# Kernel tuning notes

Hardware: AMD Instinct MI355X
Metric: run time of the kernel (lower is better)

The kernel has to match this reference:

```python
import jax, jax.numpy as jnp
import numpy as np

N = 50000      # nodes
E = 800000     # edges (avg degree 16)
NF, EF, H, OUT, K = 16, 8, 64, 8, 3
N_MID = 2      # n_gnn_layers=4 -> first + 2 mid + last


def setup_inputs() -> dict:
    key = jax.random.key(0)
    ks = jax.random.split(key, 16)
    s = 0.05
    return {
        "x": jax.random.normal(ks[0], (N, NF), dtype=jnp.float32),
        "edge_index": jax.random.randint(ks[1], (2, E), 0, N, dtype=jnp.int64),
        "edge_attr": jax.random.normal(ks[2], (E, EF), dtype=jnp.float32),
        # edge_aggr MLP: Linear(EF,H) -> ReLU -> Linear(H,1)
        "mlp_W1": jax.random.normal(ks[3], (EF, H), dtype=jnp.float32) * s,
        "mlp_b1": jnp.zeros((H,), dtype=jnp.float32),
        "mlp_W2": jax.random.normal(ks[4], (H, 1), dtype=jnp.float32) * s,
        "mlp_b2": jnp.zeros((1,), dtype=jnp.float32),
        # TAGConv-style layers: K+1 linear maps each
        "W_first": jax.random.normal(ks[5], (K + 1, NF, H), dtype=jnp.float32) * s,
        "b_first": jnp.zeros((H,), dtype=jnp.float32),
        "W_mid": jax.random.normal(ks[6], (N_MID, K + 1, H, H), dtype=jnp.float32) * s,
        "b_mid": jnp.zeros((N_MID, H), dtype=jnp.float32),
        "W_last": jax.random.normal(ks[7], (K + 1, H, OUT), dtype=jnp.float32) * s,
        "b_last": jnp.zeros((OUT,), dtype=jnp.float32),
    }


def _gcn_norm(edge_weight, src, dst, n_nodes):
    # deg computed at target (col), D^{-1/2} A D^{-1/2}, no self loops
    deg = jax.ops.segment_sum(edge_weight, dst, num_segments=n_nodes)
    dinv = jnp.where(deg > 0, jax.lax.rsqrt(jnp.where(deg > 0, deg, 1.0)), 0.0)
    return dinv[src] * edge_weight * dinv[dst]  # [E]


def _tag_conv(x, Ws, b, src, dst, norm, n_nodes):
    # out = sum_k (A_norm^k x) W_k + b
    out = x @ Ws[0]
    h = x
    for k in range(1, Ws.shape[0]):
        h = jax.ops.segment_sum(h[src] * norm[:, None], dst, num_segments=n_nodes)
        out = out + h @ Ws[k]
    return out + b


def reference(x, edge_index, edge_attr, mlp_W1, mlp_b1, mlp_W2, mlp_b2,
              W_first, b_first, W_mid, b_mid, W_last, b_last):
    src, dst = edge_index[0], edge_index[1]
    n_nodes = x.shape[0]
    # edge MLP -> scalar edge weight per edge
    ew = (jax.nn.relu(edge_attr @ mlp_W1 + mlp_b1) @ mlp_W2 + mlp_b2)[:, 0]  # [E]
    norm = _gcn_norm(ew, src, dst, n_nodes)
    h = jax.nn.relu(_tag_conv(x, W_first, b_first, src, dst, norm, n_nodes))
    for i in range(W_mid.shape[0]):
        h = jax.nn.relu(_tag_conv(h, W_mid[i], b_mid[i], src, dst, norm, n_nodes))
    return _tag_conv(h, W_last, b_last, src, dst, norm, n_nodes)
```

## Files before the change

kernel.cpp:

```cpp
#include <hip/hip_runtime.h>
#include <stdint.h>

#define N_NODES 50000
#define N_EDGES 800000
#define NFEAT   16
#define EFEAT   8
#define HID     64
#define OUTF    8
#define NMID    2
#define NX      (N_NODES * NFEAT)
#define NPW     16
#define CAP     64
#define PGB     ((N_NODES + 4 * NPW - 1) / (4 * NPW))
#define PPB     ((N_NODES + 15) / 16)
#define NWB     ((N_NODES + 3) / 4)

typedef unsigned short ushort_t;
typedef unsigned int   uint_t;
typedef unsigned long long ull_t;
typedef __bf16 bf16x8 __attribute__((ext_vector_type(8)));
typedef float  f32x4  __attribute__((ext_vector_type(4)));

__device__ __forceinline__ float b2f(ushort_t u) {
    return __uint_as_float(((uint_t)u) << 16);
}
__device__ __forceinline__ ushort_t f2b(float f) {
    uint_t u = __float_as_uint(f);
    return (ushort_t)((u + 0x7fffu + ((u >> 16) & 1u)) >> 16);
}
__device__ __forceinline__ float h2f(ushort_t u) {
    union { ushort_t u; _Float16 h; } c; c.u = u; return (float)c.h;
}
__device__ __forceinline__ ushort_t f2h(float f) {
    union { ushort_t u; _Float16 h; } c; c.h = (_Float16)f; return c.u;
}

__global__ __launch_bounds__(256) void edge_mlp_kernel(
    const float* __restrict__ ea, const float* __restrict__ x,
    const int* __restrict__ ei,
    const float* __restrict__ W1, const float* __restrict__ b1,
    const float* __restrict__ W2, const float* __restrict__ b2,
    ushort_t* __restrict__ xb, float* __restrict__ ew,
    int* __restrict__ cnts, uint_t* __restrict__ bucket)
{
    __shared__ float W1s[EFEAT * HID];
    __shared__ float b1s[HID];
    __shared__ float W2s[HID];
    __shared__ float b2s;
    int tid = threadIdx.x;
    for (int i = tid; i < EFEAT * HID; i += 256) W1s[i] = W1[i];
    if (tid < HID) { b1s[tid] = b1[tid]; W2s[tid] = W2[tid]; }
    if (tid == 0) b2s = b2[0];
    __syncthreads();

    int e = blockIdx.x * 256 + tid;
    if (e >= N_EDGES) return;

    xb[e] = f2b(x[e]);

    float4 v0 = ((const float4*)ea)[2 * e];
    float4 v1 = ((const float4*)ea)[2 * e + 1];
    float a[8] = {v0.x, v0.y, v0.z, v0.w, v1.x, v1.y, v1.z, v1.w};

    float acc = b2s;
    #pragma unroll 4
    for (int j = 0; j < HID; ++j) {
        float h = b1s[j];
        #pragma unroll
        for (int i = 0; i < EFEAT; ++i) h = fmaf(a[i], W1s[i * HID + j], h);
        acc = fmaf(fmaxf(h, 0.f), W2s[j], acc);
    }
    ew[e] = acc;

    int d = ei[N_EDGES + e];
    int pos = atomicAdd(&cnts[d], 1);
    if (pos < CAP)
        bucket[(size_t)d * CAP + pos] = (uint_t)e;
}

__global__ __launch_bounds__(256) void degdinv_kernel(
    int* __restrict__ cnts, const uint_t* __restrict__ bucket,
    const float* __restrict__ ew, float* __restrict__ dinv)
{
    int tid = threadIdx.x;
    int n = blockIdx.x * 4 + (tid >> 6);
    int lane = tid & 63;
    if (n >= N_NODES) return;
    int c = cnts[n]; if (c > CAP) c = CAP;
    float w = 0.f;
    if (lane < c)
        w = ew[bucket[(size_t)n * CAP + lane]];
    #pragma unroll
    for (int o = 32; o; o >>= 1) w += __shfl_down(w, o, 64);
    if (lane == 0) {
        cnts[n] = c;
        dinv[n] = (w > 0.f) ? (1.f / sqrtf(w)) : 0.f;
    }
}

__global__ __launch_bounds__(256) void rescale_kernel(
    const int* __restrict__ cnts, const float* __restrict__ dinv,
    const float* __restrict__ ew, const int* __restrict__ ei,
    uint_t* __restrict__ bucket)
{
    int tid = threadIdx.x;
    int n = blockIdx.x * 4 + (tid >> 6);
    int lane = tid & 63;
    if (n >= N_NODES) return;
    int c = cnts[n];
    float dn = dinv[n];
    if (lane < c) {
        uint_t e = bucket[(size_t)n * CAP + lane];
        int s = ei[e];
        float nv = dinv[s] * ew[e] * dn;
        nv = fminf(fmaxf(nv, -60000.f), 60000.f);
        bucket[(size_t)n * CAP + lane] = (((uint_t)f2h(nv)) << 16) | (uint_t)s;
    }
}

template<int W>
__global__ __launch_bounds__(256, 6) void prop_kernel(
    const ushort_t* __restrict__ gsrc, ushort_t* __restrict__ gout,
    const int* __restrict__ cnts, const uint_t* __restrict__ bucket)
{
    int tid = threadIdx.x;
    int wv = tid >> 6, lane = tid & 63;
    int nb = (blockIdx.x * 4 + wv) * 4;
    if (nb >= N_NODES) return;

    int cv = (lane < 4) ? cnts[nb + lane] : 0;
    int c0 = __builtin_amdgcn_readlane(cv, 0);
    int c1 = __builtin_amdgcn_readlane(cv, 1);
    int c2 = __builtin_amdgcn_readlane(cv, 2);
    int c3 = __builtin_amdgcn_readlane(cv, 3);

    uint_t p0 = 0, p1 = 0, p2 = 0, p3 = 0;
    if (lane < c0) p0 = bucket[(size_t)(nb + 0) * CAP + lane];
    if (lane < c1) p1 = bucket[(size_t)(nb + 1) * CAP + lane];
    if (lane < c2) p2 = bucket[(size_t)(nb + 2) * CAP + lane];
    if (lane < c3) p3 = bucket[(size_t)(nb + 3) * CAP + lane];

    if (W == 64) {
        float s[4][4];
        #pragma unroll
        for (int n = 0; n < 4; ++n)
            #pragma unroll
            for (int k = 0; k < 4; ++k) s[n][k] = 0.f;

        int cq0 = c0 & ~3, cq1 = c1 & ~3, cq2 = c2 & ~3, cq3 = c3 & ~3;
        int cqm = max(max(cq0, cq1), max(cq2, cq3));

        for (int j = 0; j < cqm; j += 4) {
            #define GATHER4(pN, cqN, n)                                              \
                if (j < cqN) {                                                       \
                    _Pragma("unroll")                                                \
                    for (int k = 0; k < 4; ++k) {                                    \
                        int pe = __builtin_amdgcn_readlane((int)pN, j + k);          \
                        float nv = h2f((ushort_t)(((uint_t)pe) >> 16));              \
                        float h = b2f(gsrc[(size_t)(pe & 0xffff) * 64 + lane]);      \
                        s[n][k] = fmaf(h, nv, s[n][k]);                              \
                    }                                                                \
                }
            GATHER4(p0, cq0, 0)
            GATHER4(p1, cq1, 1)
            GATHER4(p2, cq2, 2)
            GATHER4(p3, cq3, 3)
            #undef GATHER4
        }
        #define TAIL(pN, cqN, cN, n)                                                 \
            for (int j = cqN; j < cN; ++j) {                                         \
                int pe = __builtin_amdgcn_readlane((int)pN, j);                      \
                float nv = h2f((ushort_t)(((uint_t)pe) >> 16));                      \
                float h = b2f(gsrc[(size_t)(pe & 0xffff) * 64 + lane]);              \
                s[n][0] = fmaf(h, nv, s[n][0]);                                      \
            }
        TAIL(p0, cq0, c0, 0)
        TAIL(p1, cq1, c1, 1)
        TAIL(p2, cq2, c2, 2)
        TAIL(p3, cq3, c3, 3)
        #undef TAIL

        #pragma unroll
        for (int n = 0; n < 4; ++n) {
            float v = (s[n][0] + s[n][1]) + (s[n][2] + s[n][3]);
            gout[(size_t)(nb + n) * 64 + lane] = f2b(v);
        }
    } else {
        const int il = lane & 15;
        const int quad = lane >> 4;
        #define PROC16(pN, cN, n)                                                    \
            {                                                                        \
                float s = 0.f;                                                       \
                for (int j = 0; j < cN; j += 4) {                                    \
                    int j4 = j + quad;                                               \
                    int pw = __shfl((int)pN, j4 & 63, 64);                           \
                    bool valid = j4 < cN;                                            \
                    int src = valid ? (pw & 0xffff) : 0;                             \
                    float nv = valid ? h2f((ushort_t)(((uint_t)pw) >> 16)) : 0.f;    \
                    float h = b2f(gsrc[(size_t)src * 16 + il]);                      \
                    s = fmaf(h, nv, s);                                              \
                }                                                                    \
                s += __shfl_xor(s, 16, 64);                                          \
                s += __shfl_xor(s, 32, 64);                                          \
                if (lane < 16) gout[(size_t)(nb + n) * 16 + lane] = f2b(s);          \
            }
        PROC16(p0, c0, 0)
        PROC16(p1, c1, 1)
        PROC16(p2, c2, 2)
        PROC16(p3, c3, 3)
        #undef PROC16
    }
}

template<int F32OUT>
__global__ __launch_bounds__(256, 8) void prop8_kernel(
    const ushort_t* __restrict__ gsrc, int GS, int GO,
    const ushort_t* __restrict__ add, int AS, int AO,
    ushort_t* __restrict__ outb, float* __restrict__ outf,
    const int* __restrict__ cnts, const uint_t* __restrict__ bucket)
{
    int tid = threadIdx.x;
    int wv = tid >> 6, lane = tid & 63;
    int nb = (blockIdx.x * 4 + wv) * 4;
    if (nb >= N_NODES) return;
    const int oct = lane >> 3, il = lane & 7;

    int cv = (lane < 4) ? cnts[nb + lane] : 0;
    int c0 = __builtin_amdgcn_readlane(cv, 0);
    int c1 = __builtin_amdgcn_readlane(cv, 1);
    int c2 = __builtin_amdgcn_readlane(cv, 2);
    int c3 = __builtin_amdgcn_readlane(cv, 3);

    uint_t p0 = 0, p1 = 0, p2 = 0, p3 = 0;
    if (lane < c0) p0 = bucket[(size_t)(nb + 0) * CAP + lane];
    if (lane < c1) p1 = bucket[(size_t)(nb + 1) * CAP + lane];
    if (lane < c2) p2 = bucket[(size_t)(nb + 2) * CAP + lane];
    if (lane < c3) p3 = bucket[(size_t)(nb + 3) * CAP + lane];

    #define PROC8(pN, cN, n)                                                         \
        {                                                                            \
            float s = 0.f;                                                           \
            for (int j = 0; j < cN; j += 8) {                                        \
                int jo = j + oct;                                                    \
                int pw = __shfl((int)pN, jo & 63, 64);                               \
                bool valid = jo < cN;                                                \
                int src = valid ? (pw & 0xffff) : 0;                                 \
                float nv = valid ? h2f((ushort_t)(((uint_t)pw) >> 16)) : 0.f;        \
                float h = b2f(gsrc[(size_t)src * GS + GO + il]);                     \
                s = fmaf(h, nv, s);                                                  \
            }                                                                        \
            s += __shfl_xor(s, 8, 64);                                               \
            s += __shfl_xor(s, 16, 64);                                              \
            s += __shfl_xor(s, 32, 64);                                              \
            if (lane < 8) {                                                          \
                float v = s + b2f(add[(size_t)(nb + n) * AS + AO + lane]);           \
                if (F32OUT) outf[(size_t)(nb + n) * 8 + lane] = v;                   \
                else        outb[(size_t)(nb + n) * 8 + lane] = f2b(v);              \
            }                                                                        \
        }
    PROC8(p0, c0, 0)
    PROC8(p1, c1, 1)
    PROC8(p2, c2, 2)
    PROC8(p3, c3, 3)
    #undef PROC8
}

template<int SRCW, int COUT, int ACT>
__global__ __launch_bounds__(256, 4) void gemm4_kernel(
    const ushort_t* __restrict__ s0, const ushort_t* __restrict__ s1,
    const ushort_t* __restrict__ s2, const ushort_t* __restrict__ s3,
    const float* __restrict__ Wg,
    const float* __restrict__ bias,
    ushort_t* __restrict__ outb)
{
    constexpr int NCH = (SRCW == 16) ? 2 : 8;
    constexpr int NT  = (COUT + 15) / 16;
    __shared__ __align__(16) ushort_t Bp[NCH * NT * 512];

    int tid = threadIdx.x;
    for (int idx = tid; idx < NCH * NT * 512; idx += 256) {
        int f = idx >> 9;
        int l = (idx >> 3) & 63, j = idx & 7;
        int ch = f / NT, nt = f - ch * NT;
        int kk = ((l >> 4) << 3) + j;
        int n = nt * 16 + (l & 15);
        int widx, krow;
        if (SRCW == 16) { widx = 2 * ch + (kk >> 4); krow = kk & 15; }
        else            { widx = ch >> 1;            krow = ((ch & 1) << 5) + kk; }
        float v = (n < COUT) ? Wg[((size_t)widx * SRCW + krow) * COUT + n] : 0.f;
        Bp[idx] = f2b(v);
    }
    __syncthreads();

    int wv = tid >> 6, lane = tid & 63;
    int node_base = (blockIdx.x * 4 + wv) * NPW;
    if (node_base >= N_NODES) return;
    int m = lane & 15, quad = lane >> 4;

    const ushort_t* srcs[4] = {s0, s1, s2, s3};
    bf16x8 a[NCH];
    #pragma unroll
    for (int ch = 0; ch < NCH; ++ch) {
        const ushort_t* sp;
        size_t off;
        if (SRCW == 16) {
            sp = (quad < 2) ? srcs[2 * ch] : srcs[2 * ch + 1];
            off = (size_t)(node_base + m) * 16 + (quad & 1) * 8;
        } else {
            sp = srcs[ch >> 1];
            off = (size_t)(node_base + m) * 64 + ((ch & 1) << 5) + quad * 8;
        }
        a[ch] = *(const bf16x8*)(sp + off);
    }

    #pragma unroll
    for (int nt = 0; nt < NT; ++nt) {
        float bv = bias[(nt * 16 + m) & (COUT - 1)];
        f32x4 c = {bv, bv, bv, bv};
        #pragma unroll
        for (int ch = 0; ch < NCH; ++ch) {
            bf16x8 b = *(const bf16x8*)&Bp[((ch * NT + nt) * 64 + lane) * 8];
            c = __builtin_amdgcn_mfma_f32_16x16x32_bf16(a[ch], b, c, 0, 0, 0);
        }
        #pragma unroll
        for (int r = 0; r < 4; ++r) {
            int row = node_base + quad * 4 + r;
            float v = ACT ? fmaxf(c[r], 0.f) : c[r];
            outb[(size_t)row * COUT + nt * 16 + m] = f2b(v);
        }
    }
}

__global__ __launch_bounds__(256, 4) void gemmL_kernel(
    const ushort_t* __restrict__ src,
    const float* __restrict__ Wl,
    const float* __restrict__ bl,
    ushort_t* __restrict__ Z)
{
    __shared__ __align__(16) ushort_t Bp[2 * 2 * 512];

    int tid = threadIdx.x;
    for (int idx = tid; idx < 2048; idx += 256) {
        int f = idx >> 9;
        int ch = f >> 1, nt = f & 1;
        int l = (idx >> 3) & 63, j = idx & 7;
        int kg = ch * 32 + ((l >> 4) << 3) + j;
        int n = nt * 16 + (l & 15);
        int widx = n >> 3, col = n & 7;
        Bp[idx] = f2b(Wl[((size_t)widx * 64 + kg) * 8 + col]);
    }
    __syncthreads();

    int wv = tid >> 6, lane = tid & 63;
    int node_base = (blockIdx.x * 4 + wv) * NPW;
    if (node_base >= N_NODES) return;
    int m = lane & 15, quad = lane >> 4;

    bf16x8 a[2];
    #pragma unroll
    for (int ch = 0; ch < 2; ++ch)
        a[ch] = *(const bf16x8*)(src + (size_t)(node_base + m) * 64 + ch * 32 + quad * 8);

    #pragma unroll
    for (int nt = 0; nt < 2; ++nt) {
        int n = nt * 16 + m;
        float bv = (n < 8) ? bl[n] : 0.f;
        f32x4 c = {bv, bv, bv, bv};
        #pragma unroll
        for (int ch = 0; ch < 2; ++ch) {
            bf16x8 b = *(const bf16x8*)&Bp[((ch * 2 + nt) * 64 + lane) * 8];
            c = __builtin_amdgcn_mfma_f32_16x16x32_bf16(a[ch], b, c, 0, 0, 0);
        }
        #pragma unroll
        for (int r = 0; r < 4; ++r) {
            int row = node_base + quad * 4 + r;
            Z[(size_t)row * 32 + n] = f2b(c[r]);
        }
    }
}

extern "C" void kernel_launch(void* const* d_in, const int* in_sizes, int n_in,
                              void* d_out, int out_size, void* d_ws, size_t ws_size,
                              hipStream_t stream)
{
    const float* x  = (const float*)d_in[0];
    const int*   ei = (const int*)d_in[1];
    const float* ea = (const float*)d_in[2];
    const float* W1 = (const float*)d_in[3];
    const float* b1 = (const float*)d_in[4];
    const float* W2 = (const float*)d_in[5];
    const float* b2 = (const float*)d_in[6];
    const float* Wf = (const float*)d_in[7];
    const float* bf = (const float*)d_in[8];
    const float* Wm = (const float*)d_in[9];
    const float* bm = (const float*)d_in[10];
    const float* Wl = (const float*)d_in[11];
    const float* bl = (const float*)d_in[12];

    char* ws = (char*)d_ws;
    size_t off = 0;
    auto take = [&](size_t bytes) -> char* {
        char* p = ws + off;
        off = (off + bytes + 255) & ~(size_t)255;
        return p;
    };
    int*      cnts   = (int*)take((size_t)N_NODES * 4);
    float*    dinv   = (float*)take((size_t)N_NODES * 4);
    float*    ew     = (float*)take((size_t)N_EDGES * 4);
    uint_t*   bucket = (uint_t*)take((size_t)N_NODES * CAP * 4);
    ushort_t* xb     = (ushort_t*)take((size_t)NX * 2 + 256);
    ushort_t* g1     = (ushort_t*)take((size_t)N_NODES * HID * 2 + 256);
    ushort_t* g2     = (ushort_t*)take((size_t)N_NODES * HID * 2 + 256);
    ushort_t* g3     = (ushort_t*)take((size_t)N_NODES * HID * 2 + 256);
    ushort_t* curA   = (ushort_t*)take((size_t)N_NODES * HID * 2 + 256);
    ushort_t* curB   = (ushort_t*)take((size_t)N_NODES * HID * 2 + 256);
    ushort_t* Z      = (ushort_t*)take((size_t)N_NODES * 32 * 2 + 256);
    ushort_t* t8a    = (ushort_t*)take((size_t)N_NODES * 8 * 2 + 256);
    ushort_t* t8b    = (ushort_t*)take((size_t)N_NODES * 8 * 2 + 256);

    hipMemsetAsync(cnts, 0, (size_t)N_NODES * 4, stream);

    const int EB = (N_EDGES + 255) / 256;

    edge_mlp_kernel<<<EB, 256, 0, stream>>>(ea, x, ei, W1, b1, W2, b2, xb, ew, cnts, bucket);
    degdinv_kernel<<<NWB, 256, 0, stream>>>(cnts, bucket, ew, dinv);
    rescale_kernel<<<NWB, 256, 0, stream>>>(cnts, dinv, ew, ei, bucket);

    prop_kernel<NFEAT><<<PPB, 256, 0, stream>>>(xb, g1, cnts, bucket);
    prop_kernel<NFEAT><<<PPB, 256, 0, stream>>>(g1, g2, cnts, bucket);
    prop_kernel<NFEAT><<<PPB, 256, 0, stream>>>(g2, g3, cnts, bucket);
    gemm4_kernel<NFEAT, HID, 1><<<PGB, 256, 0, stream>>>(
        xb, g1, g2, g3, Wf, bf, curA);

    ushort_t* cin = curA;
    ushort_t* cot = curB;
    for (int L = 0; L < NMID; ++L) {
        prop_kernel<HID><<<PPB, 256, 0, stream>>>(cin, g1, cnts, bucket);
        prop_kernel<HID><<<PPB, 256, 0, stream>>>(g1, g2, cnts, bucket);
        prop_kernel<HID><<<PPB, 256, 0, stream>>>(g2, g3, cnts, bucket);
        gemm4_kernel<HID, HID, 1><<<PGB, 256, 0, stream>>>(
            cin, g1, g2, g3, Wm + (size_t)L * 4 * HID * HID, bm + L * HID, cot);
        ushort_t* t = cin; cin = cot; cot = t;
    }

    gemmL_kernel<<<PGB, 256, 0, stream>>>(cin, Wl, bl, Z);
    prop8_kernel<0><<<PPB, 256, 0, stream>>>(Z, 32, 24, Z, 32, 16, t8a, nullptr, cnts, bucket);
    prop8_kernel<0><<<PPB, 256, 0, stream>>>(t8a, 8, 0, Z, 32, 8, t8b, nullptr, cnts, bucket);
    prop8_kernel<1><<<PPB, 256, 0, stream>>>(t8b, 8, 0, Z, 32, 0, nullptr, (float*)d_out, cnts, bucket);
}
```

Baseline: 456.3 us.

## Fuse third mid-layer propagation hop with the 4-way GEMM and transpose edge-MLP weights

For each middle layer, the third propagation hop is fused with the four-term MFMA GEMM into one kernel. The gathered hop-3 features are staged in shared memory instead of being written to and re-read from a global buffer, which removes one kernel launch per layer. The cost is that each block of 16 nodes rebuilds the full 64x256 weight panel in LDS, and the lower occupancy bound may hurt latency hiding for the gather. The edge MLP weights are also transposed so each hidden unit's inputs load as float4 vectors, with the bias and W2 packed into one float2.

```diff
diff --git a/kernel.cpp b/kernel.cpp
--- a/kernel.cpp
+++ b/kernel.cpp
@@ -43,13 +43,15 @@
     ushort_t* __restrict__ xb, float* __restrict__ ew,
     int* __restrict__ cnts, uint_t* __restrict__ bucket)
 {
-    __shared__ float W1s[EFEAT * HID];
-    __shared__ float b1s[HID];
-    __shared__ float W2s[HID];
+    __shared__ __align__(16) float W1t[EFEAT * HID];
+    __shared__ __align__(8)  float2 b1w2[HID];
     __shared__ float b2s;
     int tid = threadIdx.x;
-    for (int i = tid; i < EFEAT * HID; i += 256) W1s[i] = W1[i];
-    if (tid < HID) { b1s[tid] = b1[tid]; W2s[tid] = W2[tid]; }
+    for (int idx = tid; idx < EFEAT * HID; idx += 256) {
+        int j = idx >> 3, i = idx & 7;
+        W1t[idx] = W1[i * HID + j];
+    }
+    if (tid < HID) b1w2[tid] = make_float2(b1[tid], W2[tid]);
     if (tid == 0) b2s = b2[0];
     __syncthreads();
 
@@ -60,15 +62,19 @@
 
     float4 v0 = ((const float4*)ea)[2 * e];
     float4 v1 = ((const float4*)ea)[2 * e + 1];
-    float a[8] = {v0.x, v0.y, v0.z, v0.w, v1.x, v1.y, v1.z, v1.w};
 
     float acc = b2s;
-    #pragma unroll 4
+    #pragma unroll 2
     for (int j = 0; j < HID; ++j) {
-        float h = b1s[j];
-        #pragma unroll
-        for (int i = 0; i < EFEAT; ++i) h = fmaf(a[i], W1s[i * HID + j], h);
-        acc = fmaf(fmaxf(h, 0.f), W2s[j], acc);
+        float4 wa = *(const float4*)&W1t[j * 8];
+        float4 wb = *(const float4*)&W1t[j * 8 + 4];
+        float2 bw = b1w2[j];
+        float h = bw.x;
+        h = fmaf(v0.x, wa.x, h); h = fmaf(v0.y, wa.y, h);
+        h = fmaf(v0.z, wa.z, h); h = fmaf(v0.w, wa.w, h);
+        h = fmaf(v1.x, wb.x, h); h = fmaf(v1.y, wb.y, h);
+        h = fmaf(v1.z, wb.z, h); h = fmaf(v1.w, wb.w, h);
+        acc = fmaf(fmaxf(h, 0.f), bw.y, acc);
     }
     ew[e] = acc;
 
@@ -118,6 +124,51 @@
     }
 }
 
+#define GATHER_PROLOG(WROW)                                                          \
+    int cv = (lane < 4) ? cnts[nb + lane] : 0;                                       \
+    int c0 = __builtin_amdgcn_readlane(cv, 0);                                       \
+    int c1 = __builtin_amdgcn_readlane(cv, 1);                                       \
+    int c2 = __builtin_amdgcn_readlane(cv, 2);                                       \
+    int c3 = __builtin_amdgcn_readlane(cv, 3);                                       \
+    uint_t p0 = 0, p1 = 0, p2 = 0, p3 = 0;                                           \
+    if (lane < c0) p0 = bucket[(size_t)(nb + 0) * CAP + lane];                       \
+    if (lane < c1) p1 = bucket[(size_t)(nb + 1) * CAP + lane];                       \
+    if (lane < c2) p2 = bucket[(size_t)(nb + 2) * CAP + lane];                       \
+    if (lane < c3) p3 = bucket[(size_t)(nb + 3) * CAP + lane];
+
+#define GATHER64_BODY()                                                              \
+    float s[4][4];                                                                   \
+    _Pragma("unroll")                                                                \
+    for (int n = 0; n < 4; ++n) {                                                    \
+        _Pragma("unroll")                                                            \
+        for (int k = 0; k < 4; ++k) s[n][k] = 0.f;                                   \
+    }                                                                                \
+    int cq0 = c0 & ~3, cq1 = c1 & ~3, cq2 = c2 & ~3, cq3 = c3 & ~3;                  \
+    int cqm = max(max(cq0, cq1), max(cq2, cq3));                                     \
+    for (int j = 0; j < cqm; j += 4) {                                               \
+        GAT4(p0, cq0, 0) GAT4(p1, cq1, 1) GAT4(p2, cq2, 2) GAT4(p3, cq3, 3)          \
+    }                                                                                \
+    TAILG(p0, cq0, c0, 0) TAILG(p1, cq1, c1, 1)                                      \
+    TAILG(p2, cq2, c2, 2) TAILG(p3, cq3, c3, 3)
+
+#define GAT4(pN, cqN, n)                                                             \
+    if (j < cqN) {                                                                   \
+        _Pragma("unroll")                                                            \
+        for (int k = 0; k < 4; ++k) {                                                \
+            int pe = __builtin_amdgcn_readlane((int)pN, j + k);                      \
+            float nv = h2f((ushort_t)(((uint_t)pe) >> 16));                          \
+            float h = b2f(gsrc[(size_t)(pe & 0xffff) * 64 + lane]);                  \
+            s[n][k] = fmaf(h, nv, s[n][k]);                                          \
+        }                                                                            \
+    }
+#define TAILG(pN, cqN, cN, n)                                                        \
+    for (int j = cqN; j < cN; ++j) {                                                 \
+        int pe = __builtin_amdgcn_readlane((int)pN, j);                              \
+        float nv = h2f((ushort_t)(((uint_t)pe) >> 16));                              \
+        float h = b2f(gsrc[(size_t)(pe & 0xffff) * 64 + lane]);                      \
+        s[n][0] = fmaf(h, nv, s[n][0]);                                              \
+    }
+
 template<int W>
 __global__ __launch_bounds__(256, 6) void prop_kernel(
     const ushort_t* __restrict__ gsrc, ushort_t* __restrict__ gout,
@@ -128,58 +179,10 @@
     int nb = (blockIdx.x * 4 + wv) * 4;
     if (nb >= N_NODES) return;
 
-    int cv = (lane < 4) ? cnts[nb + lane] : 0;
-    int c0 = __builtin_amdgcn_readlane(cv, 0);
-    int c1 = __builtin_amdgcn_readlane(cv, 1);
-    int c2 = __builtin_amdgcn_readlane(cv, 2);
-    int c3 = __builtin_amdgcn_readlane(cv, 3);
-
-    uint_t p0 = 0, p1 = 0, p2 = 0, p3 = 0;
-    if (lane < c0) p0 = bucket[(size_t)(nb + 0) * CAP + lane];
-    if (lane < c1) p1 = bucket[(size_t)(nb + 1) * CAP + lane];
-    if (lane < c2) p2 = bucket[(size_t)(nb + 2) * CAP + lane];
-    if (lane < c3) p3 = bucket[(size_t)(nb + 3) * CAP + lane];
+    GATHER_PROLOG(W)
 
     if (W == 64) {
-        float s[4][4];
-        #pragma unroll
-        for (int n = 0; n < 4; ++n)
-            #pragma unroll
-            for (int k = 0; k < 4; ++k) s[n][k] = 0.f;
-
-        int cq0 = c0 & ~3, cq1 = c1 & ~3, cq2 = c2 & ~3, cq3 = c3 & ~3;
-        int cqm = max(max(cq0, cq1), max(cq2, cq3));
-
-        for (int j = 0; j < cqm; j += 4) {
-            #define GATHER4(pN, cqN, n)                                              \
-                if (j < cqN) {                                                       \
-                    _Pragma("unroll")                                                \
-                    for (int k = 0; k < 4; ++k) {                                    \
-                        int pe = __builtin_amdgcn_readlane((int)pN, j + k);          \
-                        float nv = h2f((ushort_t)(((uint_t)pe) >> 16));              \
-                        float h = b2f(gsrc[(size_t)(pe & 0xffff) * 64 + lane]);      \
-                        s[n][k] = fmaf(h, nv, s[n][k]);                              \
-                    }                                                                \
-                }
-            GATHER4(p0, cq0, 0)
-            GATHER4(p1, cq1, 1)
-            GATHER4(p2, cq2, 2)
-            GATHER4(p3, cq3, 3)
-            #undef GATHER4
-        }
-        #define TAIL(pN, cqN, cN, n)                                                 \
-            for (int j = cqN; j < cN; ++j) {                                         \
-                int pe = __builtin_amdgcn_readlane((int)pN, j);                      \
-                float nv = h2f((ushort_t)(((uint_t)pe) >> 16));                      \
-                float h = b2f(gsrc[(size_t)(pe & 0xffff) * 64 + lane]);              \
-                s[n][0] = fmaf(h, nv, s[n][0]);                                      \
-            }
-        TAIL(p0, cq0, c0, 0)
-        TAIL(p1, cq1, c1, 1)
-        TAIL(p2, cq2, c2, 2)
-        TAIL(p3, cq3, c3, 3)
-        #undef TAIL
-
+        GATHER64_BODY()
         #pragma unroll
         for (int n = 0; n < 4; ++n) {
             float v = (s[n][0] + s[n][1]) + (s[n][2] + s[n][3]);
@@ -212,6 +215,71 @@
     }
 }
 
+__global__ __launch_bounds__(256, 4) void propg_kernel(
+    const ushort_t* __restrict__ g2in,
+    const ushort_t* __restrict__ s0,
+    const ushort_t* __restrict__ s1,
+    const float* __restrict__ Wg,
+    const float* __restrict__ bias,
+    ushort_t* __restrict__ outb,
+    const int* __restrict__ cnts, const uint_t* __restrict__ bucket)
+{
+    __shared__ __align__(16) ushort_t Bp[8 * 4 * 512];
+    __shared__ __align__(16) ushort_t gt[16 * 72];
+
+    int tid = threadIdx.x;
+    for (int idx = tid; idx < 8 * 4 * 512; idx += 256) {
+        int f = idx >> 9;
+        int ch = f >> 2, nt = f & 3;
+        int l = (idx >> 3) & 63, j = idx & 7;
+        int kk = ((l >> 4) << 3) + j;
+        int n = nt * 16 + (l & 15);
+        int widx = ch >> 1, krow = ((ch & 1) << 5) + kk;
+        Bp[idx] = f2b(Wg[((size_t)widx * 64 + krow) * 64 + n]);
+    }
+
+    int wv = tid >> 6, lane = tid & 63;
+    int nb = blockIdx.x * 16 + wv * 4;
+    const ushort_t* gsrc = g2in;
+
+    GATHER_PROLOG(64)
+    GATHER64_BODY()
+    #pragma unroll
+    for (int n = 0; n < 4; ++n) {
+        float v = (s[n][0] + s[n][1]) + (s[n][2] + s[n][3]);
+        gt[(wv * 4 + n) * 72 + lane] = f2b(v);
+    }
+    __syncthreads();
+
+    int m = lane & 15, quad = lane >> 4;
+    bf16x8 a[8];
+    #pragma unroll
+    for (int ch = 0; ch < 8; ++ch) {
+        int widx = ch >> 1, kh = ch & 1;
+        if (widx == 0)
+            a[ch] = *(const bf16x8*)(s0 + (size_t)(blockIdx.x * 16 + m) * 64 + kh * 32 + quad * 8);
+        else if (widx == 1)
+            a[ch] = *(const bf16x8*)(s1 + (size_t)(blockIdx.x * 16 + m) * 64 + kh * 32 + quad * 8);
+        else if (widx == 2)
+            a[ch] = *(const bf16x8*)(g2in + (size_t)(blockIdx.x * 16 + m) * 64 + kh * 32 + quad * 8);
+        else
+            a[ch] = *(const bf16x8*)&gt[m * 72 + kh * 32 + quad * 8];
+    }
+
+    float bv = bias[wv * 16 + m];
+    f32x4 c = {bv, bv, bv, bv};
+    #pragma unroll
+    for (int ch = 0; ch < 8; ++ch) {
+        bf16x8 b = *(const bf16x8*)&Bp[((ch * 4 + wv) * 64 + lane) * 8];
+        c = __builtin_amdgcn_mfma_f32_16x16x32_bf16(a[ch], b, c, 0, 0, 0);
+    }
+    #pragma unroll
+    for (int r = 0; r < 4; ++r) {
+        int row = blockIdx.x * 16 + quad * 4 + r;
+        outb[(size_t)row * 64 + wv * 16 + m] = f2b(fmaxf(c[r], 0.f));
+    }
+}
+
 template<int F32OUT>
 __global__ __launch_bounds__(256, 8) void prop8_kernel(
     const ushort_t* __restrict__ gsrc, int GS, int GO,
@@ -225,17 +293,7 @@
     if (nb >= N_NODES) return;
     const int oct = lane >> 3, il = lane & 7;
 
-    int cv = (lane < 4) ? cnts[nb + lane] : 0;
-    int c0 = __builtin_amdgcn_readlane(cv, 0);
-    int c1 = __builtin_amdgcn_readlane(cv, 1);
-    int c2 = __builtin_amdgcn_readlane(cv, 2);
-    int c3 = __builtin_amdgcn_readlane(cv, 3);
-
-    uint_t p0 = 0, p1 = 0, p2 = 0, p3 = 0;
-    if (lane < c0) p0 = bucket[(size_t)(nb + 0) * CAP + lane];
-    if (lane < c1) p1 = bucket[(size_t)(nb + 1) * CAP + lane];
-    if (lane < c2) p2 = bucket[(size_t)(nb + 2) * CAP + lane];
-    if (lane < c3) p3 = bucket[(size_t)(nb + 3) * CAP + lane];
+    GATHER_PROLOG(8)
 
     #define PROC8(pN, cN, n)                                                         \
         {                                                                            \
@@ -269,8 +327,7 @@
 __global__ __launch_bounds__(256, 4) void gemm4_kernel(
     const ushort_t* __restrict__ s0, const ushort_t* __restrict__ s1,
     const ushort_t* __restrict__ s2, const ushort_t* __restrict__ s3,
-    const float* __restrict__ Wg,
-    const float* __restrict__ bias,
+    const float* __restrict__ Wg, const float* __restrict__ bias,
     ushort_t* __restrict__ outb)
 {
     constexpr int NCH = (SRCW == 16) ? 2 : 8;
@@ -333,8 +390,7 @@
 
 __global__ __launch_bounds__(256, 4) void gemmL_kernel(
     const ushort_t* __restrict__ src,
-    const float* __restrict__ Wl,
-    const float* __restrict__ bl,
+    const float* __restrict__ Wl, const float* __restrict__ bl,
     ushort_t* __restrict__ Z)
 {
     __shared__ __align__(16) ushort_t Bp[2 * 2 * 512];
@@ -437,9 +493,8 @@
     for (int L = 0; L < NMID; ++L) {
         prop_kernel<HID><<<PPB, 256, 0, stream>>>(cin, g1, cnts, bucket);
         prop_kernel<HID><<<PPB, 256, 0, stream>>>(g1, g2, cnts, bucket);
-        prop_kernel<HID><<<PPB, 256, 0, stream>>>(g2, g3, cnts, bucket);
-        gemm4_kernel<HID, HID, 1><<<PGB, 256, 0, stream>>>(
-            cin, g1, g2, g3, Wm + (size_t)L * 4 * HID * HID, bm + L * HID, cot);
+        propg_kernel<<<PPB, 256, 0, stream>>>(
+            g2, cin, g1, Wm + (size_t)L * 4 * HID * HID, bm + L * HID, cot, cnts, bucket);
         ushort_t* t = cin; cin = cot; cot = t;
     }
 
```

Measured after the change: 580.3 us. +27.2%, slower.
